# Kernel tuning notes

Measured on AMD Instinct MI355X. Metric: run time of the kernel, lower is better.

Reference implementation:

```python
import jax, jax.numpy as jnp
import numpy as np

B, S, H, T, NF = 64, 512, 1024, 4, 12
P = NF * (NF - 1) // 2  # 66 step pairs


def _head(x, w1, b1, w2, b2):
    # LinearsHead (eval mode: dropout = identity): linear -> relu -> linear
    return jax.nn.relu(x @ w1 + b1) @ w2 + b2


def setup_inputs() -> dict:
    key = jax.random.key(0)
    ks = jax.random.split(key, 12)
    sc = 0.02
    # non-overlapping contiguous spans: targets then facts, each L tokens
    L = S // (T + NF)  # 32
    t_start = jnp.arange(T, dtype=jnp.int32) * L
    f_start = (T + jnp.arange(NF, dtype=jnp.int32)) * L
    target_offsets = jnp.broadcast_to(jnp.stack([t_start, t_start + L], -1), (B, T, 2))
    fact_offsets = jnp.broadcast_to(jnp.stack([f_start, f_start + L], -1), (B, NF, 2))
    return {
        'seq_features': jax.random.normal(ks[0], (B, S, H), jnp.float32),
        'cls_features': jax.random.normal(ks[1], (B, H), jnp.float32),
        'target_offsets': target_offsets,
        'fact_offsets': fact_offsets,
        'fact_score_mask': jnp.ones((B, NF, T), jnp.float32),
        'sentsim_w1': sc * jax.random.normal(ks[2], (2 * H, H), jnp.float32),
        'sentsim_b1': jnp.zeros((H,), jnp.float32),
        'sentsim_w2': sc * jax.random.normal(ks[3], (H, 1), jnp.float32),
        'sentsim_b2': jnp.zeros((1,), jnp.float32),
        'step_w1': sc * jax.random.normal(ks[4], (2 * H, H), jnp.float32),
        'step_b1': jnp.zeros((H,), jnp.float32),
        'step_w2': sc * jax.random.normal(ks[5], (H, 1), jnp.float32),
        'step_b2': jnp.zeros((1,), jnp.float32),
        'state_w1': sc * jax.random.normal(ks[6], (H, H), jnp.float32),
        'state_b1': jnp.zeros((H,), jnp.float32),
        'state_w2': sc * jax.random.normal(ks[7], (H, 1), jnp.float32),
        'state_b2': jnp.zeros((1,), jnp.float32),
        'abd_w1': sc * jax.random.normal(ks[8], (2 * H, H), jnp.float32),
        'abd_b1': jnp.zeros((H,), jnp.float32),
        'abd_w2': sc * jax.random.normal(ks[9], (H, 1), jnp.float32),
        'abd_b2': jnp.zeros((1,), jnp.float32),
        'lambda_weight': jnp.array([0.5, 0.5], jnp.float32),
    }


def reference(seq_features, cls_features, target_offsets, fact_offsets, fact_score_mask,
              sentsim_w1, sentsim_b1, sentsim_w2, sentsim_b2,
              step_w1, step_b1, step_w2, step_b2,
              state_w1, state_b1, state_w2, state_b2,
              abd_w1, abd_b1, abd_w2, abd_b2, lambda_weight):
    b, s, h = seq_features.shape
    t = target_offsets.shape[1]
    nf = fact_offsets.shape[1]
    pos = jnp.arange(s)

    def seg_mean(offs):  # offs [b,k,2] -> mean-pooled [b,k,h]
        m = ((pos >= offs[..., 0:1]) & (pos < offs[..., 1:2])).astype(seq_features.dtype)
        cnt = (offs[..., 1] - offs[..., 0]).astype(seq_features.dtype)[..., None]
        return jnp.einsum('bks,bsh->bkh', m, seq_features) / cnt

    tgt = seg_mean(target_offsets)  # [b,t,h]
    fct = seg_mean(fact_offsets)    # [b,nf,h]

    # fact-cls pairs ordered target-major: features[ti*nf+fi] = cat(fact, target)
    ff = jnp.broadcast_to(fct[:, None], (b, t, nf, h))
    tt = jnp.broadcast_to(tgt[:, :, None], (b, t, nf, h))
    pair = jnp.concatenate([ff, tt], -1).reshape(b, t * nf, 2 * h)
    fact_score = jax.nn.sigmoid(_head(pair, sentsim_w1, sentsim_b1, sentsim_w2, sentsim_b2)[..., 0])  # [b, t*nf]
    # original does .view(len(facts), len(targets)) on the flat t-major scores
    mat = fact_score.reshape(b, nf, t)
    max_per_fact = jnp.max(mat * fact_score_mask, axis=2)  # [b, nf]
    state_fact = jnp.mean(max_per_fact, axis=1)            # [b]
    state_cls = jax.nn.sigmoid(_head(cls_features, state_w1, state_b1, state_w2, state_b2)[..., 0])
    w = jax.nn.softmax(lambda_weight)
    state = w[0] * state_fact + w[1] * state_cls           # [b]

    # step pairs: combinations(range(nf), 2) == row-major triu indices
    i1, i2 = jnp.triu_indices(nf, k=1)
    step_feat = jnp.concatenate([fct[:, i1], fct[:, i2]], -1)  # [b,P,2h]
    step = _head(step_feat, step_w1, step_b1, step_w2, step_b2)[..., 0]  # [b,P]

    tside = jnp.mean(tgt, axis=1)  # sum/len over targets [b,h]
    abd_feat = jnp.concatenate([jnp.broadcast_to(tside[:, None], (b, nf, h)), fct], -1)
    abd = _head(abd_feat, abd_w1, abd_b1, abd_w2, abd_b2)[..., 0]  # [b,nf]

    # step_func == 'softmax_all': joint softmax over step + abd scores
    allsc = jax.nn.softmax(jnp.concatenate([step, abd], axis=1), axis=1)
    np_pairs = i1.shape[0]
    step, abd = allsc[:, :np_pairs], allsc[:, np_pairs:]

    # pack: [state | fact_score | step | step_abd]
    return jnp.concatenate([state[:, None], fact_score, step, abd], axis=1)
```

## Files before the change

### kernel.cpp

```cpp
#include <hip/hip_runtime.h>
#include <hip/hip_bf16.h>

#define B_    64
#define S_    512
#define H_    1024
#define HH_   (H_*H_)
#define T_    4
#define NF_   12
#define TNF_  48
#define NP_   66
#define OUTC_ 127

#define NSENT_ (B_*TNF_)
#define NSTEP_ (B_*NP_)
#define NABD_  (B_*NF_)
#define NCLS_  (B_)
#define NWAVES_ (NSENT_+NSTEP_+NABD_+NCLS_)

#define AROW_FCT   0
#define AROW_TGT   768
#define AROW_TSD   1024
#define AROW_CLS   1088
#define AROWS_PAD_ 1280

#define GROW_FSENT 0
#define GROW_S1    768
#define GROW_S2    1536
#define GROW_AF    2304
#define GROW_TSENT 3072
#define GROW_AT    3328
#define GROW_CLS   3392
#define GROWS_     3456

typedef __bf16 bf16x8 __attribute__((ext_vector_type(8)));
typedef float  f32x4  __attribute__((ext_vector_type(4)));
typedef __attribute__((address_space(1))) const unsigned int gcu32;
typedef __attribute__((address_space(3))) unsigned int lu32;

__device__ __forceinline__ ushort f2bf(float x) {
    union { float f; unsigned u; } c; c.f = x;
    unsigned r = c.u + 0x7fffu + ((c.u >> 16) & 1u);
    return (ushort)(r >> 16);
}
__device__ __forceinline__ float bflo(unsigned u) {
    union { unsigned u; float f; } c; c.u = u << 16; return c.f;
}
__device__ __forceinline__ float bfhi(unsigned u) {
    union { unsigned u; float f; } c; c.u = u & 0xffff0000u; return c.f;
}

__global__ __launch_bounds__(256) void prep_kernel(
    const float* __restrict__ seq, const int* __restrict__ toffs,
    const int* __restrict__ foffs, const float* __restrict__ cls,
    const float* __restrict__ sw1, const float* __restrict__ pw1,
    const float* __restrict__ aw1, const float* __restrict__ cw1,
    float* __restrict__ tgt32, ushort* __restrict__ Abf,
    ushort* __restrict__ Wt)
{
    int blk = blockIdx.x;
    int tid = threadIdx.x;

    if (blk < 1024) {
        int b = blk >> 4;
        int k = blk & 15;
        int start, end, arow;
        float* dst32 = nullptr;
        if (k < T_) {
            start = toffs[(b*T_ + k)*2];
            end   = toffs[(b*T_ + k)*2 + 1];
            dst32 = tgt32 + (size_t)(b*T_ + k) * H_;
            arow  = AROW_TGT + b*T_ + k;
        } else {
            int f = k - T_;
            start = foffs[(b*NF_ + f)*2];
            end   = foffs[(b*NF_ + f)*2 + 1];
            arow  = AROW_FCT + b*NF_ + f;
        }
        int h0 = tid * 4;
        const float* base = seq + ((size_t)b * S_ + start) * H_ + h0;
        float4 s = make_float4(0.f, 0.f, 0.f, 0.f);
        int n = end - start;
        #pragma unroll 4
        for (int r = 0; r < n; ++r) {
            float4 v = *(const float4*)(base + (size_t)r * H_);
            s.x += v.x; s.y += v.y; s.z += v.z; s.w += v.w;
        }
        float inv = 1.f / (float)n;
        s.x *= inv; s.y *= inv; s.z *= inv; s.w *= inv;
        if (dst32) *(float4*)(dst32 + h0) = s;
        ushort4 q; q.x = f2bf(s.x); q.y = f2bf(s.y); q.z = f2bf(s.z); q.w = f2bf(s.w);
        *(ushort4*)(Abf + (size_t)arow * H_ + h0) = q;
    } else if (blk < 1088) {
        int b = blk - 1024;
        int h0 = tid * 4;
        float4 c = *(const float4*)(cls + (size_t)b * H_ + h0);
        ushort4 qc; qc.x = f2bf(c.x); qc.y = f2bf(c.y); qc.z = f2bf(c.z); qc.w = f2bf(c.w);
        *(ushort4*)(Abf + (size_t)(AROW_CLS + b) * H_ + h0) = qc;
    } else {
        __shared__ float Tt[32][33];
        int idx2 = blk - 1088;
        int z = idx2 >> 10;
        int rem = idx2 & 1023;
        int k0 = (rem >> 5) * 32;
        int n0 = (rem & 31) * 32;
        const float* src;
        switch (z) {
            case 0: src = sw1; break;
            case 1: src = pw1; break;
            case 2: src = pw1 + HH_; break;
            case 3: src = aw1 + HH_; break;
            case 4: src = sw1 + HH_; break;
            case 5: src = aw1; break;
            default: src = cw1; break;
        }
        int ty = tid >> 3, tx = tid & 7;
        float4 v = *(const float4*)(src + (size_t)(k0 + ty) * H_ + n0 + tx*4);
        Tt[ty][tx*4 + 0] = v.x; Tt[ty][tx*4 + 1] = v.y;
        Tt[ty][tx*4 + 2] = v.z; Tt[ty][tx*4 + 3] = v.w;
        __syncthreads();
        int nx = ty, kx = tx;
        ushort4 q;
        q.x = f2bf(Tt[kx*4 + 0][nx]); q.y = f2bf(Tt[kx*4 + 1][nx]);
        q.z = f2bf(Tt[kx*4 + 2][nx]); q.w = f2bf(Tt[kx*4 + 3][nx]);
        *(ushort4*)(Wt + (size_t)z * HH_ + (size_t)(n0 + nx) * H_ + k0 + kx*4) = q;
    }
}

__global__ __launch_bounds__(256) void tside_kernel(
    const float* __restrict__ tgt32, ushort* __restrict__ Abf)
{
    int b = blockIdx.x;
    int h0 = threadIdx.x * 4;
    float4 s = make_float4(0.f, 0.f, 0.f, 0.f);
    for (int t = 0; t < T_; ++t) {
        float4 v = *(const float4*)(tgt32 + (size_t)(b*T_ + t)*H_ + h0);
        s.x += v.x; s.y += v.y; s.z += v.z; s.w += v.w;
    }
    ushort4 q;
    q.x = f2bf(s.x*0.25f); q.y = f2bf(s.y*0.25f);
    q.z = f2bf(s.z*0.25f); q.w = f2bf(s.w*0.25f);
    *(ushort4*)(Abf + (size_t)(AROW_TSD + b) * H_ + h0) = q;
}

__global__ __launch_bounds__(256) void gemm_bf16_kernel(
    const ushort* __restrict__ Abf, const ushort* __restrict__ Wt,
    ushort* __restrict__ G)
{
    __shared__ __align__(16) ushort As[4][128*32];
    __shared__ __align__(16) ushort Bs[4][128*32];

    const int id = blockIdx.x;
    int arow_base, wsel, grow_base, m0, vrows, by;
    if (id < 192) {
        int j = id / 48, r = id % 48, mt = r >> 3;
        by = r & 7;
        arow_base = AROW_FCT; wsel = j; grow_base = j * 768;
        m0 = mt * 128; vrows = 128;
    } else if (id < 208) {
        int r = id - 192; int mtt = r >> 3; by = r & 7;
        arow_base = AROW_TGT; wsel = 4; grow_base = GROW_TSENT;
        m0 = mtt * 128; vrows = 128;
    } else if (id < 216) {
        by = id & 7;
        arow_base = AROW_TSD; wsel = 5; grow_base = GROW_AT; m0 = 0; vrows = 64;
    } else {
        by = id & 7;
        arow_base = AROW_CLS; wsel = 6; grow_base = GROW_CLS; m0 = 0; vrows = 64;
    }

    const int tid  = threadIdx.x;
    const int lane = tid & 63;
    const int w    = tid >> 6;
    const int wr   = w >> 1, wc = w & 1;
    const int n0   = by * 128;

    const int srow = lane >> 2;
    const int scol = ((lane & 3) ^ ((lane >> 3) & 3)) * 8;
    const ushort* gA0 = Abf + (size_t)(arow_base + m0 + w*16 + srow) * H_ + scol;
    const ushort* gA1 = gA0 + (size_t)64 * H_;
    const ushort* gB0 = Wt + (size_t)wsel * HH_
                        + (size_t)(n0 + w*16 + srow) * H_ + scol;
    const ushort* gB1 = gB0 + (size_t)64 * H_;
    const int ldsA0 = (0*64 + w*16) * 32, ldsA1 = (1*64 + w*16) * 32;

    const int frr  = lane & 15;
    const int c0   = lane >> 4;
    const int swz  = (frr >> 1) & 3;
    const int offA = (wr*64 + frr) * 32 + (c0 ^ swz) * 8;
    const int offB = (wc*64 + frr) * 32 + (c0 ^ swz) * 8;

    f32x4 acc[4][4];
    #pragma unroll
    for (int i = 0; i < 4; ++i)
        #pragma unroll
        for (int j = 0; j < 4; ++j)
            acc[i][j] = (f32x4){0.f, 0.f, 0.f, 0.f};

    #define STAGE(buf, kstep) do {                                              \
        int kk_ = (kstep) * 32;                                                 \
        __builtin_amdgcn_global_load_lds((gcu32*)(gA0 + kk_),                   \
            (lu32*)(As[buf] + ldsA0), 16, 0, 0);                                \
        __builtin_amdgcn_global_load_lds((gcu32*)(gA1 + kk_),                   \
            (lu32*)(As[buf] + ldsA1), 16, 0, 0);                                \
        __builtin_amdgcn_global_load_lds((gcu32*)(gB0 + kk_),                   \
            (lu32*)(Bs[buf] + ldsA0), 16, 0, 0);                                \
        __builtin_amdgcn_global_load_lds((gcu32*)(gB1 + kk_),                   \
            (lu32*)(Bs[buf] + ldsA1), 16, 0, 0);                                \
    } while (0)

    #define COMPUTE(cur) do {                                                   \
        const ushort* pa = As[cur] + offA;                                      \
        const ushort* pb = Bs[cur] + offB;                                      \
        bf16x8 a0 = *(const bf16x8*)(pa);                                       \
        bf16x8 a1 = *(const bf16x8*)(pa + 16*32);                               \
        bf16x8 a2 = *(const bf16x8*)(pa + 32*32);                               \
        bf16x8 a3 = *(const bf16x8*)(pa + 48*32);                               \
        bf16x8 b0 = *(const bf16x8*)(pb);                                       \
        bf16x8 b1 = *(const bf16x8*)(pb + 16*32);                               \
        bf16x8 b2 = *(const bf16x8*)(pb + 32*32);                               \
        bf16x8 b3 = *(const bf16x8*)(pb + 48*32);                               \
        asm volatile("s_waitcnt lgkmcnt(0)" ::: "memory");                      \
        __builtin_amdgcn_sched_barrier(0);                                      \
        bf16x8 av[4] = {a0, a1, a2, a3};                                        \
        bf16x8 bv[4] = {b0, b1, b2, b3};                                        \
        _Pragma("unroll")                                                       \
        for (int i = 0; i < 4; ++i)                                             \
            _Pragma("unroll")                                                   \
            for (int j = 0; j < 4; ++j)                                         \
                acc[i][j] = __builtin_amdgcn_mfma_f32_16x16x32_bf16(            \
                    av[i], bv[j], acc[i][j], 0, 0, 0);                          \
    } while (0)

    STAGE(0, 0);
    STAGE(1, 1);
    STAGE(2, 2);

    #pragma unroll 1
    for (int t = 0; t < 30; ++t) {
        asm volatile("s_waitcnt vmcnt(8)" ::: "memory");
        __builtin_amdgcn_s_barrier();
        __builtin_amdgcn_sched_barrier(0);
        if (t < 29) STAGE((t + 3) & 3, t + 3);
        COMPUTE(t & 3);
    }
    asm volatile("s_waitcnt vmcnt(4)" ::: "memory");
    __builtin_amdgcn_s_barrier();
    __builtin_amdgcn_sched_barrier(0);
    COMPUTE(2);
    asm volatile("s_waitcnt vmcnt(0)" ::: "memory");
    __builtin_amdgcn_s_barrier();
    __builtin_amdgcn_sched_barrier(0);
    COMPUTE(3);

    #undef STAGE
    #undef COMPUTE

    const int r0 = (lane >> 4) * 4;
    const int cc = lane & 15;
    #pragma unroll
    for (int i = 0; i < 4; ++i) {
        int lrow = wr*64 + i*16 + r0;
        if (lrow >= vrows) continue;
        #pragma unroll
        for (int r = 0; r < 4; ++r) {
            size_t gr = (size_t)(grow_base + m0 + lrow + r) * H_ + n0 + wc*64 + cc;
            #pragma unroll
            for (int j = 0; j < 4; ++j)
                G[gr + j*16] = f2bf(acc[i][j][r]);
        }
    }
}

__global__ __launch_bounds__(256) void combine_kernel(
    const ushort* __restrict__ G,
    const float* __restrict__ sb1, const float* __restrict__ sw2,
    const float* __restrict__ pb1, const float* __restrict__ pw2,
    const float* __restrict__ ab1, const float* __restrict__ aw2,
    const float* __restrict__ cb1, const float* __restrict__ cw2,
    float* __restrict__ ssent, float* __restrict__ sstep,
    float* __restrict__ sabd, float* __restrict__ scls)
{
    int wv = blockIdx.x * 4 + (threadIdx.x >> 6);
    int lane = threadIdx.x & 63;
    if (wv >= NWAVES_) return;

    const ushort *U, *V;
    const float *b1, *w2;
    float* outp;
    if (wv < NSENT_) {
        int b = wv / TNF_, q = wv % TNF_;
        int t = q / NF_, f = q % NF_;
        U = G + (size_t)(GROW_FSENT + b*NF_ + f) * H_;
        V = G + (size_t)(GROW_TSENT + b*T_ + t) * H_;
        b1 = sb1; w2 = sw2; outp = ssent + wv;
    } else if (wv < NSENT_ + NSTEP_) {
        int s = wv - NSENT_;
        int b = s / NP_, p = s % NP_;
        int i = 0, rem = p, cnt = NF_ - 1;
        while (rem >= cnt) { rem -= cnt; --cnt; ++i; }
        int j = i + 1 + rem;
        U = G + (size_t)(GROW_S1 + b*NF_ + i) * H_;
        V = G + (size_t)(GROW_S2 + b*NF_ + j) * H_;
        b1 = pb1; w2 = pw2; outp = sstep + s;
    } else if (wv < NSENT_ + NSTEP_ + NABD_) {
        int s = wv - NSENT_ - NSTEP_;
        int b = s / NF_, f = s % NF_;
        U = G + (size_t)(GROW_AT + b) * H_;
        V = G + (size_t)(GROW_AF + b*NF_ + f) * H_;
        b1 = ab1; w2 = aw2; outp = sabd + s;
    } else {
        int b = wv - NSENT_ - NSTEP_ - NABD_;
        U = G + (size_t)(GROW_CLS + b) * H_;
        V = nullptr;
        b1 = cb1; w2 = cw2; outp = scls + b;
    }

    float acc = 0.f;
    #pragma unroll
    for (int h = 0; h < 2; ++h) {
        int nb = h * 512 + lane * 8;
        uint4 uu = *(const uint4*)(U + nb);
        float us[8] = { bflo(uu.x), bfhi(uu.x), bflo(uu.y), bfhi(uu.y),
                        bflo(uu.z), bfhi(uu.z), bflo(uu.w), bfhi(uu.w) };
        if (V) {
            uint4 vv = *(const uint4*)(V + nb);
            us[0] += bflo(vv.x); us[1] += bfhi(vv.x);
            us[2] += bflo(vv.y); us[3] += bfhi(vv.y);
            us[4] += bflo(vv.z); us[5] += bfhi(vv.z);
            us[6] += bflo(vv.w); us[7] += bfhi(vv.w);
        }
        float4 bA = *(const float4*)(b1 + nb);
        float4 bB = *(const float4*)(b1 + nb + 4);
        float4 wA = *(const float4*)(w2 + nb);
        float4 wB = *(const float4*)(w2 + nb + 4);
        acc = fmaf(fmaxf(us[0] + bA.x, 0.f), wA.x, acc);
        acc = fmaf(fmaxf(us[1] + bA.y, 0.f), wA.y, acc);
        acc = fmaf(fmaxf(us[2] + bA.z, 0.f), wA.z, acc);
        acc = fmaf(fmaxf(us[3] + bA.w, 0.f), wA.w, acc);
        acc = fmaf(fmaxf(us[4] + bB.x, 0.f), wB.x, acc);
        acc = fmaf(fmaxf(us[5] + bB.y, 0.f), wB.y, acc);
        acc = fmaf(fmaxf(us[6] + bB.z, 0.f), wB.z, acc);
        acc = fmaf(fmaxf(us[7] + bB.w, 0.f), wB.w, acc);
    }
    #pragma unroll
    for (int msk = 1; msk < 64; msk <<= 1)
        acc += __shfl_xor(acc, msk);
    if (lane == 0) *outp = acc;
}

__global__ __launch_bounds__(128) void finalize_kernel(
    const float* __restrict__ s_sent, const float* __restrict__ s_step,
    const float* __restrict__ s_abd, const float* __restrict__ s_cls,
    const float* __restrict__ mask, const float* __restrict__ lam,
    const float* __restrict__ sent_b2, const float* __restrict__ step_b2,
    const float* __restrict__ state_b2, const float* __restrict__ abd_b2,
    float* __restrict__ out)
{
    int b = blockIdx.x;
    int tid = threadIdx.x;
    __shared__ float fs[TNF_];
    __shared__ float sc[NP_ + NF_];
    __shared__ float mpf[NF_];
    __shared__ float smax, ssum;

    if (tid < TNF_) {
        float v = 1.f / (1.f + expf(-(s_sent[b*TNF_ + tid] + sent_b2[0])));
        fs[tid] = v;
        out[(size_t)b*OUTC_ + 1 + tid] = v;
    }
    if (tid < NP_)
        sc[tid] = s_step[b*NP_ + tid] + step_b2[0];
    else if (tid < NP_ + NF_)
        sc[tid] = s_abd[b*NF_ + (tid - NP_)] + abd_b2[0];
    __syncthreads();

    if (tid < NF_) {
        float m = -1e30f;
        for (int j = 0; j < T_; ++j)
            m = fmaxf(m, fs[tid*T_ + j] * mask[((size_t)b*NF_ + tid)*T_ + j]);
        mpf[tid] = m;
    }
    __syncthreads();

    if (tid == 0) {
        float sf = 0.f;
        for (int i = 0; i < NF_; ++i) sf += mpf[i];
        sf *= (1.f / NF_);
        float scls2 = 1.f / (1.f + expf(-(s_cls[b] + state_b2[0])));
        float l0 = lam[0], l1 = lam[1];
        float mx = fmaxf(l0, l1);
        float e0 = expf(l0 - mx), e1 = expf(l1 - mx);
        float w0 = e0 / (e0 + e1);
        out[(size_t)b*OUTC_] = w0 * sf + (1.f - w0) * scls2;
        float m2 = -1e30f;
        for (int i = 0; i < NP_ + NF_; ++i) m2 = fmaxf(m2, sc[i]);
        smax = m2;
    }
    __syncthreads();
    if (tid < NP_ + NF_) sc[tid] = expf(sc[tid] - smax);
    __syncthreads();
    if (tid == 0) {
        float s2 = 0.f;
        for (int i = 0; i < NP_ + NF_; ++i) s2 += sc[i];
        ssum = s2;
    }
    __syncthreads();
    if (tid < NP_ + NF_)
        out[(size_t)b*OUTC_ + 1 + TNF_ + tid] = sc[tid] / ssum;
}

extern "C" void kernel_launch(void* const* d_in, const int* in_sizes, int n_in,
                              void* d_out, int out_size, void* d_ws, size_t ws_size,
                              hipStream_t stream)
{
    (void)in_sizes; (void)n_in; (void)out_size; (void)ws_size;
    const float* seq  = (const float*)d_in[0];
    const float* cls  = (const float*)d_in[1];
    const int*   toff = (const int*)d_in[2];
    const int*   foff = (const int*)d_in[3];
    const float* mask = (const float*)d_in[4];
    const float* sw1  = (const float*)d_in[5];
    const float* sb1  = (const float*)d_in[6];
    const float* sw2  = (const float*)d_in[7];
    const float* sb2  = (const float*)d_in[8];
    const float* pw1  = (const float*)d_in[9];
    const float* pb1  = (const float*)d_in[10];
    const float* pw2  = (const float*)d_in[11];
    const float* pb2  = (const float*)d_in[12];
    const float* cw1  = (const float*)d_in[13];
    const float* cb1  = (const float*)d_in[14];
    const float* cw2  = (const float*)d_in[15];
    const float* cb2  = (const float*)d_in[16];
    const float* aw1  = (const float*)d_in[17];
    const float* ab1  = (const float*)d_in[18];
    const float* aw2  = (const float*)d_in[19];
    const float* ab2  = (const float*)d_in[20];
    const float* lam  = (const float*)d_in[21];

    char* wsb = (char*)d_ws;
    float*  tgt32 = (float*)wsb;
    float*  ssent = (float*)(wsb + (1u<<20));
    float*  sstep = ssent + NSENT_;
    float*  sabd  = sstep + NSTEP_;
    float*  scls  = sabd + NABD_;
    ushort* Abf   = (ushort*)(wsb + (1u<<20) + 32768);
    ushort* Wt    = Abf + (size_t)AROWS_PAD_ * H_;
    ushort* G     = Wt + (size_t)7 * HH_;

    prep_kernel<<<1088 + 7*1024, 256, 0, stream>>>(
        seq, toff, foff, cls, sw1, pw1, aw1, cw1, tgt32, Abf, Wt);

    tside_kernel<<<B_, 256, 0, stream>>>(tgt32, Abf);

    gemm_bf16_kernel<<<224, 256, 0, stream>>>(Abf, Wt, G);

    combine_kernel<<<(NWAVES_ + 3) / 4, 256, 0, stream>>>(
        G, sb1, sw2, pb1, pw2, ab1, aw2, cb1, cw2,
        ssent, sstep, sabd, scls);

    finalize_kernel<<<B_, 128, 0, stream>>>(
        ssent, sstep, sabd, scls, mask, lam, sb2, pb2, cb2, ab2, (float*)d_out);
}
```

Before: 64.89 us.

## Split GEMM into single-wave 64x64 tiles and fuse combine with finalize

The bf16 GEMM moves from 224 four-wave blocks with 128x128 tiles to 864 single-wave blocks with 64x64 tiles and a three-buffer LDS pipeline, which removes the per-step block barriers and fills more of the CUs. The separate combine and finalize kernels become one 1024-thread kernel per batch row that keeps the head scores in shared memory instead of round-tripping through global scratch, saving one launch. The trade-off is more redundant operand loading across the smaller tiles and only 64 blocks in the fused epilogue kernel.

After: 75.84 us. +16.9%, slower.

```diff
diff --git a/kernel.cpp b/kernel.cpp
--- a/kernel.cpp
+++ b/kernel.cpp
@@ -11,17 +11,11 @@
 #define NP_   66
 #define OUTC_ 127
 
-#define NSENT_ (B_*TNF_)
-#define NSTEP_ (B_*NP_)
-#define NABD_  (B_*NF_)
-#define NCLS_  (B_)
-#define NWAVES_ (NSENT_+NSTEP_+NABD_+NCLS_)
-
 #define AROW_FCT   0
 #define AROW_TGT   768
 #define AROW_TSD   1024
 #define AROW_CLS   1088
-#define AROWS_PAD_ 1280
+#define AROWS_     1152
 
 #define GROW_FSENT 0
 #define GROW_S1    768
@@ -142,52 +136,35 @@
     *(ushort4*)(Abf + (size_t)(AROW_TSD + b) * H_ + h0) = q;
 }
 
-__global__ __launch_bounds__(256) void gemm_bf16_kernel(
+__global__ __launch_bounds__(64) void gemm_bf16_kernel(
     const ushort* __restrict__ Abf, const ushort* __restrict__ Wt,
     ushort* __restrict__ G)
 {
-    __shared__ __align__(16) ushort As[4][128*32];
-    __shared__ __align__(16) ushort Bs[4][128*32];
+    __shared__ __align__(16) ushort As[3][64*32];
+    __shared__ __align__(16) ushort Bs[3][64*32];
 
     const int id = blockIdx.x;
-    int arow_base, wsel, grow_base, m0, vrows, by;
-    if (id < 192) {
-        int j = id / 48, r = id % 48, mt = r >> 3;
-        by = r & 7;
-        arow_base = AROW_FCT; wsel = j; grow_base = j * 768;
-        m0 = mt * 128; vrows = 128;
-    } else if (id < 208) {
-        int r = id - 192; int mtt = r >> 3; by = r & 7;
-        arow_base = AROW_TGT; wsel = 4; grow_base = GROW_TSENT;
-        m0 = mtt * 128; vrows = 128;
-    } else if (id < 216) {
-        by = id & 7;
-        arow_base = AROW_TSD; wsel = 5; grow_base = GROW_AT; m0 = 0; vrows = 64;
-    } else {
-        by = id & 7;
-        arow_base = AROW_CLS; wsel = 6; grow_base = GROW_CLS; m0 = 0; vrows = 64;
-    }
-
-    const int tid  = threadIdx.x;
-    const int lane = tid & 63;
-    const int w    = tid >> 6;
-    const int wr   = w >> 1, wc = w & 1;
-    const int n0   = by * 128;
-
-    const int srow = lane >> 2;
-    const int scol = ((lane & 3) ^ ((lane >> 3) & 3)) * 8;
-    const ushort* gA0 = Abf + (size_t)(arow_base + m0 + w*16 + srow) * H_ + scol;
-    const ushort* gA1 = gA0 + (size_t)64 * H_;
-    const ushort* gB0 = Wt + (size_t)wsel * HH_
-                        + (size_t)(n0 + w*16 + srow) * H_ + scol;
-    const ushort* gB1 = gB0 + (size_t)64 * H_;
-    const int ldsA0 = (0*64 + w*16) * 32, ldsA1 = (1*64 + w*16) * 32;
-
-    const int frr  = lane & 15;
-    const int c0   = lane >> 4;
-    const int swz  = (frr >> 1) & 3;
-    const int offA = (wr*64 + frr) * 32 + (c0 ^ swz) * 8;
-    const int offB = (wc*64 + frr) * 32 + (c0 ^ swz) * 8;
+    const int mt = id >> 4;
+    const int ny = id & 15;
+    const int n0 = ny * 64;
+
+    int arow, wsel, grow;
+    if (mt < 48)      { wsel = mt / 12; int m = mt % 12;
+                        arow = AROW_FCT + m*64; grow = wsel*768 + m*64; }
+    else if (mt < 52) { wsel = 4; arow = AROW_TGT + (mt-48)*64;
+                        grow = GROW_TSENT + (mt-48)*64; }
+    else if (mt == 52){ wsel = 5; arow = AROW_TSD; grow = GROW_AT; }
+    else              { wsel = 6; arow = AROW_CLS; grow = GROW_CLS; }
+
+    const int lane  = threadIdx.x;
+    const int srow  = lane >> 2;
+    const int scol  = ((lane & 3) ^ ((lane >> 3) & 3)) * 8;
+    const ushort* gA = Abf + (size_t)(arow + srow) * H_ + scol;
+    const ushort* gB = Wt + (size_t)wsel * HH_ + (size_t)(n0 + srow) * H_ + scol;
+
+    const int frr = lane & 15;
+    const int c0  = lane >> 4;
+    const int fo  = frr * 32 + ((c0 ^ ((frr >> 1) & 3)) * 8);
 
     f32x4 acc[4][4];
     #pragma unroll
@@ -198,31 +175,33 @@
 
     #define STAGE(buf, kstep) do {                                              \
         int kk_ = (kstep) * 32;                                                 \
-        __builtin_amdgcn_global_load_lds((gcu32*)(gA0 + kk_),                   \
-            (lu32*)(As[buf] + ldsA0), 16, 0, 0);                                \
-        __builtin_amdgcn_global_load_lds((gcu32*)(gA1 + kk_),                   \
-            (lu32*)(As[buf] + ldsA1), 16, 0, 0);                                \
-        __builtin_amdgcn_global_load_lds((gcu32*)(gB0 + kk_),                   \
-            (lu32*)(Bs[buf] + ldsA0), 16, 0, 0);                                \
-        __builtin_amdgcn_global_load_lds((gcu32*)(gB1 + kk_),                   \
-            (lu32*)(Bs[buf] + ldsA1), 16, 0, 0);                                \
+        _Pragma("unroll")                                                       \
+        for (int r_ = 0; r_ < 4; ++r_) {                                        \
+            __builtin_amdgcn_global_load_lds(                                   \
+                (gcu32*)(gA + (size_t)(16*r_) * H_ + kk_),                      \
+                (lu32*)(As[buf] + r_*512), 16, 0, 0);                           \
+            __builtin_amdgcn_global_load_lds(                                   \
+                (gcu32*)(gB + (size_t)(16*r_) * H_ + kk_),                      \
+                (lu32*)(Bs[buf] + r_*512), 16, 0, 0);                           \
+        }                                                                       \
     } while (0)
 
-    #define COMPUTE(cur) do {                                                   \
-        const ushort* pa = As[cur] + offA;                                      \
-        const ushort* pb = Bs[cur] + offB;                                      \
-        bf16x8 a0 = *(const bf16x8*)(pa);                                       \
-        bf16x8 a1 = *(const bf16x8*)(pa + 16*32);                               \
-        bf16x8 a2 = *(const bf16x8*)(pa + 32*32);                               \
-        bf16x8 a3 = *(const bf16x8*)(pa + 48*32);                               \
-        bf16x8 b0 = *(const bf16x8*)(pb);                                       \
-        bf16x8 b1 = *(const bf16x8*)(pb + 16*32);                               \
-        bf16x8 b2 = *(const bf16x8*)(pb + 32*32);                               \
-        bf16x8 b3 = *(const bf16x8*)(pb + 48*32);                               \
+    #define COMPUTE(buf) do {                                                   \
+        const ushort* pa = As[buf] + fo;                                        \
+        const ushort* pb = Bs[buf] + fo;                                        \
+        bf16x8 av0 = *(const bf16x8*)(pa);                                      \
+        bf16x8 av1 = *(const bf16x8*)(pa + 512);                                \
+        bf16x8 av2 = *(const bf16x8*)(pa + 1024);                               \
+        bf16x8 av3 = *(const bf16x8*)(pa + 1536);                               \
+        bf16x8 bv0 = *(const bf16x8*)(pb);                                      \
+        bf16x8 bv1 = *(const bf16x8*)(pb + 512);                                \
+        bf16x8 bv2 = *(const bf16x8*)(pb + 1024);                               \
+        bf16x8 bv3 = *(const bf16x8*)(pb + 1536);                               \
         asm volatile("s_waitcnt lgkmcnt(0)" ::: "memory");                      \
         __builtin_amdgcn_sched_barrier(0);                                      \
-        bf16x8 av[4] = {a0, a1, a2, a3};                                        \
-        bf16x8 bv[4] = {b0, b1, b2, b3};                                        \
+        STAGE_NEXT;                                                             \
+        bf16x8 av[4] = {av0, av1, av2, av3};                                    \
+        bf16x8 bv[4] = {bv0, bv1, bv2, bv3};                                    \
         _Pragma("unroll")                                                       \
         for (int i = 0; i < 4; ++i)                                             \
             _Pragma("unroll")                                                   \
@@ -237,21 +216,17 @@
 
     #pragma unroll 1
     for (int t = 0; t < 30; ++t) {
-        asm volatile("s_waitcnt vmcnt(8)" ::: "memory");
-        __builtin_amdgcn_s_barrier();
-        __builtin_amdgcn_sched_barrier(0);
-        if (t < 29) STAGE((t + 3) & 3, t + 3);
-        COMPUTE(t & 3);
-    }
-    asm volatile("s_waitcnt vmcnt(4)" ::: "memory");
-    __builtin_amdgcn_s_barrier();
-    __builtin_amdgcn_sched_barrier(0);
-    COMPUTE(2);
+        asm volatile("s_waitcnt vmcnt(16)" ::: "memory");
+        #define STAGE_NEXT do { if (t < 29) STAGE(t % 3, t + 3); } while (0)
+        COMPUTE(t % 3);
+        #undef STAGE_NEXT
+    }
+    asm volatile("s_waitcnt vmcnt(8)" ::: "memory");
+    #define STAGE_NEXT do { } while (0)
+    COMPUTE(0);
     asm volatile("s_waitcnt vmcnt(0)" ::: "memory");
-    __builtin_amdgcn_s_barrier();
-    __builtin_amdgcn_sched_barrier(0);
-    COMPUTE(3);
-
+    COMPUTE(1);
+    #undef STAGE_NEXT
     #undef STAGE
     #undef COMPUTE
 
@@ -259,11 +234,9 @@
     const int cc = lane & 15;
     #pragma unroll
     for (int i = 0; i < 4; ++i) {
-        int lrow = wr*64 + i*16 + r0;
-        if (lrow >= vrows) continue;
         #pragma unroll
         for (int r = 0; r < 4; ++r) {
-            size_t gr = (size_t)(grow_base + m0 + lrow + r) * H_ + n0 + wc*64 + cc;
+            size_t gr = (size_t)(grow + i*16 + r0 + r) * H_ + n0 + cc;
             #pragma unroll
             for (int j = 0; j < 4; ++j)
                 G[gr + j*16] = f2bf(acc[i][j][r]);
@@ -271,109 +244,96 @@
     }
 }
 
-__global__ __launch_bounds__(256) void combine_kernel(
+__global__ __launch_bounds__(1024) void combfin_kernel(
     const ushort* __restrict__ G,
     const float* __restrict__ sb1, const float* __restrict__ sw2,
     const float* __restrict__ pb1, const float* __restrict__ pw2,
     const float* __restrict__ ab1, const float* __restrict__ aw2,
     const float* __restrict__ cb1, const float* __restrict__ cw2,
-    float* __restrict__ ssent, float* __restrict__ sstep,
-    float* __restrict__ sabd, float* __restrict__ scls)
-{
-    int wv = blockIdx.x * 4 + (threadIdx.x >> 6);
-    int lane = threadIdx.x & 63;
-    if (wv >= NWAVES_) return;
-
-    const ushort *U, *V;
-    const float *b1, *w2;
-    float* outp;
-    if (wv < NSENT_) {
-        int b = wv / TNF_, q = wv % TNF_;
-        int t = q / NF_, f = q % NF_;
-        U = G + (size_t)(GROW_FSENT + b*NF_ + f) * H_;
-        V = G + (size_t)(GROW_TSENT + b*T_ + t) * H_;
-        b1 = sb1; w2 = sw2; outp = ssent + wv;
-    } else if (wv < NSENT_ + NSTEP_) {
-        int s = wv - NSENT_;
-        int b = s / NP_, p = s % NP_;
-        int i = 0, rem = p, cnt = NF_ - 1;
-        while (rem >= cnt) { rem -= cnt; --cnt; ++i; }
-        int j = i + 1 + rem;
-        U = G + (size_t)(GROW_S1 + b*NF_ + i) * H_;
-        V = G + (size_t)(GROW_S2 + b*NF_ + j) * H_;
-        b1 = pb1; w2 = pw2; outp = sstep + s;
-    } else if (wv < NSENT_ + NSTEP_ + NABD_) {
-        int s = wv - NSENT_ - NSTEP_;
-        int b = s / NF_, f = s % NF_;
-        U = G + (size_t)(GROW_AT + b) * H_;
-        V = G + (size_t)(GROW_AF + b*NF_ + f) * H_;
-        b1 = ab1; w2 = aw2; outp = sabd + s;
-    } else {
-        int b = wv - NSENT_ - NSTEP_ - NABD_;
-        U = G + (size_t)(GROW_CLS + b) * H_;
-        V = nullptr;
-        b1 = cb1; w2 = cw2; outp = scls + b;
-    }
-
-    float acc = 0.f;
-    #pragma unroll
-    for (int h = 0; h < 2; ++h) {
-        int nb = h * 512 + lane * 8;
-        uint4 uu = *(const uint4*)(U + nb);
-        float us[8] = { bflo(uu.x), bfhi(uu.x), bflo(uu.y), bfhi(uu.y),
-                        bflo(uu.z), bfhi(uu.z), bflo(uu.w), bfhi(uu.w) };
-        if (V) {
-            uint4 vv = *(const uint4*)(V + nb);
-            us[0] += bflo(vv.x); us[1] += bfhi(vv.x);
-            us[2] += bflo(vv.y); us[3] += bfhi(vv.y);
-            us[4] += bflo(vv.z); us[5] += bfhi(vv.z);
-            us[6] += bflo(vv.w); us[7] += bfhi(vv.w);
-        }
-        float4 bA = *(const float4*)(b1 + nb);
-        float4 bB = *(const float4*)(b1 + nb + 4);
-        float4 wA = *(const float4*)(w2 + nb);
-        float4 wB = *(const float4*)(w2 + nb + 4);
-        acc = fmaf(fmaxf(us[0] + bA.x, 0.f), wA.x, acc);
-        acc = fmaf(fmaxf(us[1] + bA.y, 0.f), wA.y, acc);
-        acc = fmaf(fmaxf(us[2] + bA.z, 0.f), wA.z, acc);
-        acc = fmaf(fmaxf(us[3] + bA.w, 0.f), wA.w, acc);
-        acc = fmaf(fmaxf(us[4] + bB.x, 0.f), wB.x, acc);
-        acc = fmaf(fmaxf(us[5] + bB.y, 0.f), wB.y, acc);
-        acc = fmaf(fmaxf(us[6] + bB.z, 0.f), wB.z, acc);
-        acc = fmaf(fmaxf(us[7] + bB.w, 0.f), wB.w, acc);
-    }
-    #pragma unroll
-    for (int msk = 1; msk < 64; msk <<= 1)
-        acc += __shfl_xor(acc, msk);
-    if (lane == 0) *outp = acc;
-}
-
-__global__ __launch_bounds__(128) void finalize_kernel(
-    const float* __restrict__ s_sent, const float* __restrict__ s_step,
-    const float* __restrict__ s_abd, const float* __restrict__ s_cls,
     const float* __restrict__ mask, const float* __restrict__ lam,
     const float* __restrict__ sent_b2, const float* __restrict__ step_b2,
     const float* __restrict__ state_b2, const float* __restrict__ abd_b2,
     float* __restrict__ out)
 {
-    int b = blockIdx.x;
-    int tid = threadIdx.x;
+    const int b    = blockIdx.x;
+    const int tid  = threadIdx.x;
+    const int wv   = tid >> 6;
+    const int lane = tid & 63;
+
+    __shared__ float sc[OUTC_];
     __shared__ float fs[TNF_];
-    __shared__ float sc[NP_ + NF_];
     __shared__ float mpf[NF_];
     __shared__ float smax, ssum;
 
+    for (int s = wv; s < OUTC_; s += 16) {
+        const ushort *U, *V = nullptr;
+        const float *b1, *w2;
+        if (s < TNF_) {
+            int t = s / NF_, f = s % NF_;
+            U = G + (size_t)(GROW_FSENT + b*NF_ + f) * H_;
+            V = G + (size_t)(GROW_TSENT + b*T_ + t) * H_;
+            b1 = sb1; w2 = sw2;
+        } else if (s < TNF_ + NP_) {
+            int p = s - TNF_;
+            int i = 0, rem = p, cnt = NF_ - 1;
+            while (rem >= cnt) { rem -= cnt; --cnt; ++i; }
+            int j = i + 1 + rem;
+            U = G + (size_t)(GROW_S1 + b*NF_ + i) * H_;
+            V = G + (size_t)(GROW_S2 + b*NF_ + j) * H_;
+            b1 = pb1; w2 = pw2;
+        } else if (s < TNF_ + NP_ + NF_) {
+            int f = s - TNF_ - NP_;
+            U = G + (size_t)(GROW_AT + b) * H_;
+            V = G + (size_t)(GROW_AF + b*NF_ + f) * H_;
+            b1 = ab1; w2 = aw2;
+        } else {
+            U = G + (size_t)(GROW_CLS + b) * H_;
+            b1 = cb1; w2 = cw2;
+        }
+
+        int nb = lane * 16;
+        uint4 u0 = *(const uint4*)(U + nb);
+        uint4 u1 = *(const uint4*)(U + nb + 8);
+        float us[16] = {
+            bflo(u0.x), bfhi(u0.x), bflo(u0.y), bfhi(u0.y),
+            bflo(u0.z), bfhi(u0.z), bflo(u0.w), bfhi(u0.w),
+            bflo(u1.x), bfhi(u1.x), bflo(u1.y), bfhi(u1.y),
+            bflo(u1.z), bfhi(u1.z), bflo(u1.w), bfhi(u1.w) };
+        if (V) {
+            uint4 v0 = *(const uint4*)(V + nb);
+            uint4 v1 = *(const uint4*)(V + nb + 8);
+            us[0] += bflo(v0.x); us[1] += bfhi(v0.x);
+            us[2] += bflo(v0.y); us[3] += bfhi(v0.y);
+            us[4] += bflo(v0.z); us[5] += bfhi(v0.z);
+            us[6] += bflo(v0.w); us[7] += bfhi(v0.w);
+            us[8] += bflo(v1.x); us[9] += bfhi(v1.x);
+            us[10] += bflo(v1.y); us[11] += bfhi(v1.y);
+            us[12] += bflo(v1.z); us[13] += bfhi(v1.z);
+            us[14] += bflo(v1.w); us[15] += bfhi(v1.w);
+        }
+        float acc = 0.f;
+        #pragma unroll
+        for (int q = 0; q < 4; ++q) {
+            float4 bb = *(const float4*)(b1 + nb + q*4);
+            float4 ww = *(const float4*)(w2 + nb + q*4);
+            acc = fmaf(fmaxf(us[q*4+0] + bb.x, 0.f), ww.x, acc);
+            acc = fmaf(fmaxf(us[q*4+1] + bb.y, 0.f), ww.y, acc);
+            acc = fmaf(fmaxf(us[q*4+2] + bb.z, 0.f), ww.z, acc);
+            acc = fmaf(fmaxf(us[q*4+3] + bb.w, 0.f), ww.w, acc);
+        }
+        #pragma unroll
+        for (int msk = 1; msk < 64; msk <<= 1)
+            acc += __shfl_xor(acc, msk);
+        if (lane == 0) sc[s] = acc;
+    }
+    __syncthreads();
+
     if (tid < TNF_) {
-        float v = 1.f / (1.f + expf(-(s_sent[b*TNF_ + tid] + sent_b2[0])));
+        float v = 1.f / (1.f + expf(-(sc[tid] + sent_b2[0])));
         fs[tid] = v;
         out[(size_t)b*OUTC_ + 1 + tid] = v;
     }
-    if (tid < NP_)
-        sc[tid] = s_step[b*NP_ + tid] + step_b2[0];
-    else if (tid < NP_ + NF_)
-        sc[tid] = s_abd[b*NF_ + (tid - NP_)] + abd_b2[0];
-    __syncthreads();
-
+    __syncthreads();
     if (tid < NF_) {
         float m = -1e30f;
         for (int j = 0; j < T_; ++j)
@@ -381,32 +341,36 @@
         mpf[tid] = m;
     }
     __syncthreads();
-
     if (tid == 0) {
         float sf = 0.f;
         for (int i = 0; i < NF_; ++i) sf += mpf[i];
         sf *= (1.f / NF_);
-        float scls2 = 1.f / (1.f + expf(-(s_cls[b] + state_b2[0])));
+        float scls2 = 1.f / (1.f + expf(-(sc[126] + state_b2[0])));
         float l0 = lam[0], l1 = lam[1];
         float mx = fmaxf(l0, l1);
         float e0 = expf(l0 - mx), e1 = expf(l1 - mx);
         float w0 = e0 / (e0 + e1);
         out[(size_t)b*OUTC_] = w0 * sf + (1.f - w0) * scls2;
         float m2 = -1e30f;
-        for (int i = 0; i < NP_ + NF_; ++i) m2 = fmaxf(m2, sc[i]);
+        for (int i = 0; i < NP_; ++i) m2 = fmaxf(m2, sc[TNF_ + i] + step_b2[0]);
+        for (int i = 0; i < NF_; ++i) m2 = fmaxf(m2, sc[TNF_ + NP_ + i] + abd_b2[0]);
         smax = m2;
     }
     __syncthreads();
-    if (tid < NP_ + NF_) sc[tid] = expf(sc[tid] - smax);
+    __shared__ float ex[NP_ + NF_];
+    if (tid < NP_)
+        ex[tid] = expf(sc[TNF_ + tid] + step_b2[0] - smax);
+    else if (tid < NP_ + NF_)
+        ex[tid] = expf(sc[TNF_ + tid] + abd_b2[0] - smax);
     __syncthreads();
     if (tid == 0) {
         float s2 = 0.f;
-        for (int i = 0; i < NP_ + NF_; ++i) s2 += sc[i];
+        for (int i = 0; i < NP_ + NF_; ++i) s2 += ex[i];
         ssum = s2;
     }
     __syncthreads();
     if (tid < NP_ + NF_)
-        out[(size_t)b*OUTC_ + 1 + TNF_ + tid] = sc[tid] / ssum;
+        out[(size_t)b*OUTC_ + 1 + TNF_ + tid] = ex[tid] / ssum;
 }
 
 extern "C" void kernel_launch(void* const* d_in, const int* in_sizes, int n_in,
@@ -439,12 +403,8 @@
 
     char* wsb = (char*)d_ws;
     float*  tgt32 = (float*)wsb;
-    float*  ssent = (float*)(wsb + (1u<<20));
-    float*  sstep = ssent + NSENT_;
-    float*  sabd  = sstep + NSTEP_;
-    float*  scls  = sabd + NABD_;
-    ushort* Abf   = (ushort*)(wsb + (1u<<20) + 32768);
-    ushort* Wt    = Abf + (size_t)AROWS_PAD_ * H_;
+    ushort* Abf   = (ushort*)(wsb + (1u<<20));
+    ushort* Wt    = Abf + (size_t)AROWS_ * H_;
     ushort* G     = Wt + (size_t)7 * HH_;
 
     prep_kernel<<<1088 + 7*1024, 256, 0, stream>>>(
@@ -452,12 +412,9 @@
 
     tside_kernel<<<B_, 256, 0, stream>>>(tgt32, Abf);
 
-    gemm_bf16_kernel<<<224, 256, 0, stream>>>(Abf, Wt, G);
-
-    combine_kernel<<<(NWAVES_ + 3) / 4, 256, 0, stream>>>(
+    gemm_bf16_kernel<<<864, 64, 0, stream>>>(Abf, Wt, G);
+
+    combfin_kernel<<<B_, 1024, 0, stream>>>(
         G, sb1, sw2, pb1, pw2, ab1, aw2, cb1, cw2,
-        ssent, sstep, sabd, scls);
-
-    finalize_kernel<<<B_, 128, 0, stream>>>(
-        ssent, sstep, sabd, scls, mask, lam, sb2, pb2, cb2, ab2, (float*)d_out);
-}
+        mask, lam, sb2, pb2, cb2, ab2, (float*)d_out);
+}
```
